# Kernel optimization log

Hardware: AMD Instinct MI355X
Metric: run time of the kernel (lower is better)

The kernel has to match this reference:

```python
import jax, jax.numpy as jnp
import numpy as np

HEAD_SIZE = 64
NEG_INF = float('-inf')


def setup_inputs() -> dict:
    key = jax.random.key(0)
    ks = jax.random.split(key, 4)
    B, S, H, D = 8, 4096, 1024, HEAD_SIZE
    scale = 1.0 / np.sqrt(H)
    return {
        'x': jax.random.normal(ks[0], (B, S, H), dtype=jnp.float32),
        'Wq': jax.random.normal(ks[1], (H, D), dtype=jnp.float32) * scale,
        'bq': jnp.zeros((D,), dtype=jnp.float32),
        'Wk': jax.random.normal(ks[2], (H, D), dtype=jnp.float32) * scale,
        'bk': jnp.zeros((D,), dtype=jnp.float32),
        'Wv': jax.random.normal(ks[3], (H, D), dtype=jnp.float32) * scale,
        'bv': jnp.zeros((D,), dtype=jnp.float32),
    }


def reference(x, Wq, bq, Wk, bk, Wv, bv):
    # x: [B, S, H]; projections -> [B, S, D]
    B, S, H = x.shape
    q = jnp.einsum('bsh,hd->bsd', x, Wq) + bq
    k = jnp.einsum('bsh,hd->bsd', x, Wk) + bk
    v = jnp.einsum('bsh,hd->bsd', x, Wv) + bv
    # raw scores [B, S, S]
    scores = jnp.einsum('bqd,bkd->bqk', q, k)
    # causal mask applied BEFORE scaling (matches original; -inf/scale == -inf)
    causal = jnp.tril(jnp.ones((S, S), dtype=bool))
    scores = jnp.where(causal, scores, NEG_INF)
    scale = 1.0 / jnp.sqrt(jnp.asarray(q.shape[-1], dtype=scores.dtype))
    attn = jax.nn.softmax(scores * scale, axis=-1)
    # dropout = 0.0 (eval) -> identity
    return jnp.einsum('bqk,bkd->bqd', attn, v)
```

## Files before the change

### kernel.cpp

```cpp
#include <hip/hip_runtime.h>
#include <hip/hip_bf16.h>
#include <math.h>

#define SEQ 4096
#define HID 1024
#define DH  64
#define NB  8
#define QSCALE 0.18033688011112042f

typedef unsigned short ushort_t;
typedef unsigned int   uint_t;
typedef __attribute__((ext_vector_type(8))) short  bf16x8;
typedef __attribute__((ext_vector_type(4))) float  f32x4;
typedef __attribute__((ext_vector_type(4))) uint_t u32x4;
typedef __attribute__((ext_vector_type(2))) uint_t u32x2;

static __device__ __forceinline__ ushort_t f2bf(float f) {
    __hip_bfloat16 h = __float2bfloat16(f);
    return *reinterpret_cast<ushort_t*>(&h);
}
static __device__ __forceinline__ ushort_t f2bf_fast(float f) {
    uint_t u = __float_as_uint(f);
    return (ushort_t)((u + 0x8000u) >> 16);
}
static __device__ __forceinline__ uint_t bfpair(float lo, float hi) {
    return (uint_t)f2bf_fast(lo) | ((uint_t)f2bf_fast(hi) << 16);
}

static __device__ __forceinline__ void gld_lds16(const void* g, void* s) {
    __builtin_amdgcn_global_load_lds(
        (const __attribute__((address_space(1))) void*)g,
        (__attribute__((address_space(3))) void*)s, 16, 0, 0);
}

__global__ __launch_bounds__(256) void prep_w(
    const float* __restrict__ Wq, const float* __restrict__ Wk,
    const float* __restrict__ Wv, ushort_t* __restrict__ wts)
{
    __shared__ ushort_t tr[64][72];
    const int bx   = blockIdx.x;
    const int mmat = bx >> 4;
    const int kt   = bx & 15;
    const float* W  = (mmat == 0) ? Wq : (mmat == 1) ? Wk : Wv;
    const float  sc = (mmat == 0) ? QSCALE : 1.0f;

    const int t  = threadIdx.x;
    const int kr = t >> 2, kc = (t & 3) * 16;
    const float* src = W + (size_t)(kt * 64 + kr) * DH + kc;
    float4 a0 = *(const float4*)(src);
    float4 a1 = *(const float4*)(src + 4);
    float4 a2 = *(const float4*)(src + 8);
    float4 a3 = *(const float4*)(src + 12);
    float vv[16] = {a0.x,a0.y,a0.z,a0.w, a1.x,a1.y,a1.z,a1.w,
                    a2.x,a2.y,a2.z,a2.w, a3.x,a3.y,a3.z,a3.w};
    #pragma unroll
    for (int i = 0; i < 16; ++i) tr[kr][kc + i] = f2bf(vv[i] * sc);
    __syncthreads();

    const int cl = t >> 2, jc = (t & 3) * 16;
    const int c  = mmat * 64 + cl;
    ushort_t* dst = wts + kt * 12288 + c * 64;
    #pragma unroll
    for (int jj = 0; jj < 16; ++jj) {
        int j = jc + jj;
        dst[((j >> 3) ^ (cl & 7)) * 8 + (j & 7)] = tr[j][cl];
    }
}

__global__ __launch_bounds__(256) void qkv_proj(
    const float* __restrict__ x, const ushort_t* __restrict__ wts,
    const float* __restrict__ bq, const float* __restrict__ bk,
    const float* __restrict__ bv,
    ushort_t* __restrict__ qimg, ushort_t* __restrict__ kimg,
    ushort_t* __restrict__ vimg)
{
    __shared__ ushort_t xs[2][64][72];
    __shared__ ushort_t bw[2][12288];

    const int t  = threadIdx.x;
    const int w  = t >> 6, l = t & 63, lr = l & 15, lg = l >> 4;
    const int row0 = blockIdx.x * 64;
    const int sxr = t >> 2, sxc = (t & 3) * 16;
    const int ch0 = (lg ^ (lr & 7)) * 8;
    const int ch1 = ((lg + 4) ^ (lr & 7)) * 8;

    f32x4 acc[4][3];
    #pragma unroll
    for (int i = 0; i < 4; ++i)
        #pragma unroll
        for (int j = 0; j < 3; ++j) acc[i][j] = (f32x4){0.f,0.f,0.f,0.f};

    float4 Xf[4];
    u32x4  Bf[6];
    {
        const float* xr = x + (size_t)(row0 + sxr) * HID + sxc;
        Xf[0] = *(const float4*)(xr);      Xf[1] = *(const float4*)(xr + 4);
        Xf[2] = *(const float4*)(xr + 8);  Xf[3] = *(const float4*)(xr + 12);
        const char* bsrc = (const char*)wts + t * 16;
        #pragma unroll
        for (int i = 0; i < 6; ++i) Bf[i] = *(const u32x4*)(bsrc + i * 4096);
    }

    for (int kt = 0; kt < 16; ++kt) {
        const int buf = kt & 1;
        {
            u32x4 p0, p1;
            p0.x = bfpair(Xf[0].x, Xf[0].y);
            p0.y = bfpair(Xf[0].z, Xf[0].w);
            p0.z = bfpair(Xf[1].x, Xf[1].y);
            p0.w = bfpair(Xf[1].z, Xf[1].w);
            p1.x = bfpair(Xf[2].x, Xf[2].y);
            p1.y = bfpair(Xf[2].z, Xf[2].w);
            p1.z = bfpair(Xf[3].x, Xf[3].y);
            p1.w = bfpair(Xf[3].z, Xf[3].w);
            *(u32x4*)&xs[buf][sxr][sxc]     = p0;
            *(u32x4*)&xs[buf][sxr][sxc + 8] = p1;
            char* bdst = (char*)&bw[buf][0] + t * 16;
            #pragma unroll
            for (int i = 0; i < 6; ++i) *(u32x4*)(bdst + i * 4096) = Bf[i];
        }
        __syncthreads();
        if (kt < 15) {
            const float* xr = x + (size_t)(row0 + sxr) * HID + (kt + 1) * 64 + sxc;
            Xf[0] = *(const float4*)(xr);      Xf[1] = *(const float4*)(xr + 4);
            Xf[2] = *(const float4*)(xr + 8);  Xf[3] = *(const float4*)(xr + 12);
            const char* bsrc = (const char*)wts + (kt + 1) * 24576 + t * 16;
            #pragma unroll
            for (int i = 0; i < 6; ++i) Bf[i] = *(const u32x4*)(bsrc + i * 4096);
        }
        bf16x8 af0[4], af1[4];
        #pragma unroll
        for (int rt = 0; rt < 4; ++rt) {
            af0[rt] = *(bf16x8*)&xs[buf][rt * 16 + lr][lg * 8];
            af1[rt] = *(bf16x8*)&xs[buf][rt * 16 + lr][lg * 8 + 32];
        }
        #pragma unroll
        for (int ctl = 0; ctl < 3; ++ctl) {
            const int c = (w * 3 + ctl) * 16 + lr;
            bf16x8 b0 = *(bf16x8*)&bw[buf][c * 64 + ch0];
            bf16x8 b1 = *(bf16x8*)&bw[buf][c * 64 + ch1];
            #pragma unroll
            for (int rt = 0; rt < 4; ++rt) {
                acc[rt][ctl] = __builtin_amdgcn_mfma_f32_16x16x32_bf16(
                    af0[rt], b0, acc[rt][ctl], 0, 0, 0);
                acc[rt][ctl] = __builtin_amdgcn_mfma_f32_16x16x32_bf16(
                    af1[rt], b1, acc[rt][ctl], 0, 0, 0);
            }
        }
    }

    #pragma unroll
    for (int ctl = 0; ctl < 3; ++ctl) {
        const int c    = (w * 3 + ctl) * 16 + lr;
        const int mmat = c >> 6;
        const int cc   = c & 63;
        const float* bp = (mmat == 0) ? bq : (mmat == 1) ? bk : bv;
        const float bias = bp[cc] * (mmat == 0 ? QSCALE : 1.0f);
        #pragma unroll
        for (int rt = 0; rt < 4; ++rt)
            #pragma unroll
            for (int r = 0; r < 4; ++r) {
                const int s = row0 + rt * 16 + lg * 4 + r;
                const ushort_t v = f2bf(acc[rt][ctl][r] + bias);
                if (mmat == 0)
                    qimg[(size_t)s * 64 + cc] = v;
                else if (mmat == 1)
                    kimg[(size_t)(s >> 6) * 4096 + (s & 63) * 64 +
                         ((cc >> 3) ^ (s & 7)) * 8 + (cc & 7)] = v;
                else
                    vimg[(size_t)(s >> 6) * 4096 + (size_t)cc * 64 +
                         (((s & 63) >> 3) ^ (cc & 7)) * 8 + (s & 7)] = v;
            }
    }
}

__global__ __launch_bounds__(256) void attn(
    const ushort_t* __restrict__ qimg, const ushort_t* __restrict__ kimg,
    const ushort_t* __restrict__ vimg, float* __restrict__ outg)
{
    __shared__ ushort_t kvs[2][8192];
    __shared__ ushort_t ps[64][72];

    const int t  = threadIdx.x;
    const int w  = t >> 6, l = t & 63, lr = l & 15, g = l >> 4;
    const int bx = blockIdx.x;
    const int qt = (bx < 256) ? (63 - (bx >> 3)) : ((bx - 256) >> 3);
    const int b  = bx & 7;
    const int q0 = qt * 64;
    const int ch0 = (g ^ (lr & 7)) * 8;
    const int ch1 = ((g + 4) ^ (lr & 7)) * 8;
    const int qq  = q0 + w * 16 + lr;

    bf16x8 qf0, qf1;
    {
        const ushort_t* qp = qimg + (size_t)(b * SEQ + qq) * 64 + g * 8;
        qf0 = *(const bf16x8*)(qp);
        qf1 = *(const bf16x8*)(qp + 32);
    }

    f32x4 o[4];
    #pragma unroll
    for (int dt = 0; dt < 4; ++dt) o[dt] = (f32x4){0.f,0.f,0.f,0.f};
    float lpart = 0.f;

    const char* kbase = (const char*)kimg + (size_t)b * 524288;
    const char* vbase = (const char*)vimg + (size_t)b * 524288;
    const int wo = w * 1024;
    const int lo = l * 16;

    {
        char* lk = (char*)&kvs[0][0];
        gld_lds16(kbase + wo + lo,        lk + wo);
        gld_lds16(kbase + wo + lo + 4096, lk + wo + 4096);
        gld_lds16(vbase + wo + lo,        lk + wo + 8192);
        gld_lds16(vbase + wo + lo + 4096, lk + wo + 12288);
    }

    for (int kt = 0; kt <= qt; ++kt) {
        const int cur = kt & 1;
        __syncthreads();
        if (kt < qt) {
            const char* ks = kbase + (size_t)(kt + 1) * 8192;
            const char* vs = vbase + (size_t)(kt + 1) * 8192;
            char*       lk = (char*)&kvs[cur ^ 1][0];
            gld_lds16(ks + wo + lo,        lk + wo);
            gld_lds16(ks + wo + lo + 4096, lk + wo + 4096);
            gld_lds16(vs + wo + lo,        lk + wo + 8192);
            gld_lds16(vs + wo + lo + 4096, lk + wo + 12288);
        }

        const ushort_t* kb = &kvs[cur][0];
        f32x4 s[4];
        #pragma unroll
        for (int ct = 0; ct < 4; ++ct) {
            const int rowb = (ct * 16 + lr) * 64;
            bf16x8 kf0 = *(const bf16x8*)(kb + rowb + ch0);
            bf16x8 kf1 = *(const bf16x8*)(kb + rowb + ch1);
            s[ct] = (f32x4){0.f,0.f,0.f,0.f};
            s[ct] = __builtin_amdgcn_mfma_f32_16x16x32_bf16(kf0, qf0, s[ct], 0, 0, 0);
            s[ct] = __builtin_amdgcn_mfma_f32_16x16x32_bf16(kf1, qf1, s[ct], 0, 0, 0);
        }

        if (kt == qt) {
            const int kvb = kt * 64 + g * 4;
            #pragma unroll
            for (int ct = 0; ct < 4; ++ct) {
                float p0 = ((kvb + ct*16 + 0) > qq) ? 0.f : __builtin_amdgcn_exp2f(s[ct][0]);
                float p1 = ((kvb + ct*16 + 1) > qq) ? 0.f : __builtin_amdgcn_exp2f(s[ct][1]);
                float p2 = ((kvb + ct*16 + 2) > qq) ? 0.f : __builtin_amdgcn_exp2f(s[ct][2]);
                float p3 = ((kvb + ct*16 + 3) > qq) ? 0.f : __builtin_amdgcn_exp2f(s[ct][3]);
                lpart += (p0 + p1) + (p2 + p3);
                u32x2 pk = { bfpair(p0, p1), bfpair(p2, p3) };
                *(u32x2*)&ps[w * 16 + lr][ct * 16 + g * 4] = pk;
            }
        } else {
            #pragma unroll
            for (int ct = 0; ct < 4; ++ct) {
                float p0 = __builtin_amdgcn_exp2f(s[ct][0]);
                float p1 = __builtin_amdgcn_exp2f(s[ct][1]);
                float p2 = __builtin_amdgcn_exp2f(s[ct][2]);
                float p3 = __builtin_amdgcn_exp2f(s[ct][3]);
                lpart += (p0 + p1) + (p2 + p3);
                u32x2 pk = { bfpair(p0, p1), bfpair(p2, p3) };
                *(u32x2*)&ps[w * 16 + lr][ct * 16 + g * 4] = pk;
            }
        }
        asm volatile("s_waitcnt lgkmcnt(0)" ::: "memory");

        bf16x8 pf0 = *(const bf16x8*)&ps[w * 16 + lr][g * 8];
        bf16x8 pf1 = *(const bf16x8*)&ps[w * 16 + lr][32 + g * 8];
        const ushort_t* vb = &kvs[cur][4096];
        #pragma unroll
        for (int dt = 0; dt < 4; ++dt) {
            const int rowb = (dt * 16 + lr) * 64;
            bf16x8 vf0 = *(const bf16x8*)(vb + rowb + ch0);
            bf16x8 vf1 = *(const bf16x8*)(vb + rowb + ch1);
            o[dt] = __builtin_amdgcn_mfma_f32_16x16x32_bf16(vf0, pf0, o[dt], 0, 0, 0);
            o[dt] = __builtin_amdgcn_mfma_f32_16x16x32_bf16(vf1, pf1, o[dt], 0, 0, 0);
        }
    }

    lpart += __shfl_xor(lpart, 16);
    lpart += __shfl_xor(lpart, 32);
    const float inv = 1.0f / lpart;

    float* orow = outg + (size_t)(b * SEQ + qq) * 64;
    #pragma unroll
    for (int dt = 0; dt < 4; ++dt) {
        float4 val = { o[dt][0] * inv, o[dt][1] * inv,
                       o[dt][2] * inv, o[dt][3] * inv };
        *(float4*)&orow[dt * 16 + g * 4] = val;
    }
}

extern "C" void kernel_launch(void* const* d_in, const int* in_sizes, int n_in,
                              void* d_out, int out_size, void* d_ws, size_t ws_size,
                              hipStream_t stream) {
    const float* x  = (const float*)d_in[0];
    const float* Wq = (const float*)d_in[1];
    const float* bq = (const float*)d_in[2];
    const float* Wk = (const float*)d_in[3];
    const float* bk = (const float*)d_in[4];
    const float* Wv = (const float*)d_in[5];
    const float* bv = (const float*)d_in[6];
    float* out = (float*)d_out;

    const size_t per = (size_t)NB * SEQ * DH;
    ushort_t* q   = (ushort_t*)d_ws;
    ushort_t* k   = q + per;
    ushort_t* v   = k + per;
    ushort_t* wts = v + per;

    prep_w  <<<dim3(48),  256, 0, stream>>>(Wq, Wk, Wv, wts);
    qkv_proj<<<dim3(512), 256, 0, stream>>>(x, wts, bq, bk, bv, q, k, v);
    attn    <<<dim3(512), 256, 0, stream>>>(q, k, v, out);
}
```

Before: 273.4 us.

## Split attention key range across two blocks and merge partials; async weight loads

The attention kernel now splits each query tile's causal key range into two halves, each handled by a separate block (1024 blocks). Each block writes unnormalised partial outputs and row sums to workspace, and a new merge kernel adds them and normalises. The aim is better load balance and more parallelism across CUs for the long causal rows. The cost is an extra launch and extra partial-buffer traffic. Separately, the projection kernel loads weights with direct global-to-LDS copies instead of staging them in registers, and uses a cheaper bf16 rounding in its epilogue. The merge relies on a fixed softmax offset with no running max, which the code before also used, so adding the two halves' sums is consistent.

```diff
diff --git a/kernel.cpp b/kernel.cpp
--- a/kernel.cpp
+++ b/kernel.cpp
@@ -90,15 +90,18 @@
         #pragma unroll
         for (int j = 0; j < 3; ++j) acc[i][j] = (f32x4){0.f,0.f,0.f,0.f};
 
+    const char* wbase = (const char*)wts;
+    const int   wlo   = w * 1024 + l * 16;
+
     float4 Xf[4];
-    u32x4  Bf[6];
     {
         const float* xr = x + (size_t)(row0 + sxr) * HID + sxc;
         Xf[0] = *(const float4*)(xr);      Xf[1] = *(const float4*)(xr + 4);
         Xf[2] = *(const float4*)(xr + 8);  Xf[3] = *(const float4*)(xr + 12);
-        const char* bsrc = (const char*)wts + t * 16;
-        #pragma unroll
-        for (int i = 0; i < 6; ++i) Bf[i] = *(const u32x4*)(bsrc + i * 4096);
+        char* bdst = (char*)&bw[0][0] + w * 1024;
+        #pragma unroll
+        for (int i = 0; i < 6; ++i)
+            gld_lds16(wbase + wlo + i * 4096, bdst + i * 4096);
     }
 
     for (int kt = 0; kt < 16; ++kt) {
@@ -115,18 +118,17 @@
             p1.w = bfpair(Xf[3].z, Xf[3].w);
             *(u32x4*)&xs[buf][sxr][sxc]     = p0;
             *(u32x4*)&xs[buf][sxr][sxc + 8] = p1;
-            char* bdst = (char*)&bw[buf][0] + t * 16;
-            #pragma unroll
-            for (int i = 0; i < 6; ++i) *(u32x4*)(bdst + i * 4096) = Bf[i];
         }
         __syncthreads();
         if (kt < 15) {
             const float* xr = x + (size_t)(row0 + sxr) * HID + (kt + 1) * 64 + sxc;
             Xf[0] = *(const float4*)(xr);      Xf[1] = *(const float4*)(xr + 4);
             Xf[2] = *(const float4*)(xr + 8);  Xf[3] = *(const float4*)(xr + 12);
-            const char* bsrc = (const char*)wts + (kt + 1) * 24576 + t * 16;
-            #pragma unroll
-            for (int i = 0; i < 6; ++i) Bf[i] = *(const u32x4*)(bsrc + i * 4096);
+            char* bdst = (char*)&bw[buf ^ 1][0] + w * 1024;
+            const char* bsrc = wbase + (size_t)(kt + 1) * 24576 + wlo;
+            #pragma unroll
+            for (int i = 0; i < 6; ++i)
+                gld_lds16(bsrc + i * 4096, bdst + i * 4096);
         }
         bf16x8 af0[4], af1[4];
         #pragma unroll
@@ -161,7 +163,7 @@
             #pragma unroll
             for (int r = 0; r < 4; ++r) {
                 const int s = row0 + rt * 16 + lg * 4 + r;
-                const ushort_t v = f2bf(acc[rt][ctl][r] + bias);
+                const ushort_t v = f2bf_fast(acc[rt][ctl][r] + bias);
                 if (mmat == 0)
                     qimg[(size_t)s * 64 + cc] = v;
                 else if (mmat == 1)
@@ -176,17 +178,23 @@
 
 __global__ __launch_bounds__(256) void attn(
     const ushort_t* __restrict__ qimg, const ushort_t* __restrict__ kimg,
-    const ushort_t* __restrict__ vimg, float* __restrict__ outg)
+    const ushort_t* __restrict__ vimg,
+    float* __restrict__ Opart, float* __restrict__ Lpart)
 {
     __shared__ ushort_t kvs[2][8192];
     __shared__ ushort_t ps[64][72];
 
     const int t  = threadIdx.x;
     const int w  = t >> 6, l = t & 63, lr = l & 15, g = l >> 4;
-    const int bx = blockIdx.x;
-    const int qt = (bx < 256) ? (63 - (bx >> 3)) : ((bx - 256) >> 3);
-    const int b  = bx & 7;
-    const int q0 = qt * 64;
+    const int bx   = blockIdx.x;
+    const int half = bx & 1;
+    const int u    = bx >> 1;
+    const int qt   = 63 - (u >> 3);
+    const int b    = u & 7;
+    const int q0   = qt * 64;
+    const int n    = qt + 1, h = n >> 1;
+    const int t0   = half ? h : 0;
+    const int t1   = half ? n : h;
     const int ch0 = (g ^ (lr & 7)) * 8;
     const int ch1 = ((g + 4) ^ (lr & 7)) * 8;
     const int qq  = q0 + w * 16 + lr;
@@ -208,18 +216,20 @@
     const int wo = w * 1024;
     const int lo = l * 16;
 
-    {
+    if (t0 < t1) {
+        const char* ks = kbase + (size_t)t0 * 8192;
+        const char* vs = vbase + (size_t)t0 * 8192;
         char* lk = (char*)&kvs[0][0];
-        gld_lds16(kbase + wo + lo,        lk + wo);
-        gld_lds16(kbase + wo + lo + 4096, lk + wo + 4096);
-        gld_lds16(vbase + wo + lo,        lk + wo + 8192);
-        gld_lds16(vbase + wo + lo + 4096, lk + wo + 12288);
-    }
-
-    for (int kt = 0; kt <= qt; ++kt) {
-        const int cur = kt & 1;
+        gld_lds16(ks + wo + lo,        lk + wo);
+        gld_lds16(ks + wo + lo + 4096, lk + wo + 4096);
+        gld_lds16(vs + wo + lo,        lk + wo + 8192);
+        gld_lds16(vs + wo + lo + 4096, lk + wo + 12288);
+    }
+
+    for (int kt = t0; kt < t1; ++kt) {
+        const int cur = (kt - t0) & 1;
         __syncthreads();
-        if (kt < qt) {
+        if (kt + 1 < t1) {
             const char* ks = kbase + (size_t)(kt + 1) * 8192;
             const char* vs = vbase + (size_t)(kt + 1) * 8192;
             char*       lk = (char*)&kvs[cur ^ 1][0];
@@ -282,14 +292,38 @@
 
     lpart += __shfl_xor(lpart, 16);
     lpart += __shfl_xor(lpart, 32);
-    const float inv = 1.0f / lpart;
-
-    float* orow = outg + (size_t)(b * SEQ + qq) * 64;
-    #pragma unroll
-    for (int dt = 0; dt < 4; ++dt) {
-        float4 val = { o[dt][0] * inv, o[dt][1] * inv,
-                       o[dt][2] * inv, o[dt][3] * inv };
-        *(float4*)&orow[dt * 16 + g * 4] = val;
+
+    const int m = b * 64 + qt;
+    float* Op = Opart + ((size_t)half * 512 + m) * 4096;
+    #pragma unroll
+    for (int dt = 0; dt < 4; ++dt)
+        *(f32x4*)&Op[(w * 16 + lr) * 64 + dt * 16 + g * 4] = o[dt];
+    if (g == 0)
+        Lpart[((size_t)half * 512 + m) * 64 + w * 16 + lr] = lpart;
+}
+
+__global__ __launch_bounds__(256) void merge_o(
+    const float* __restrict__ Opart, const float* __restrict__ Lpart,
+    float* __restrict__ outg)
+{
+    const int m = blockIdx.x;
+    const int b = m >> 6, qt = m & 63;
+    const int t = threadIdx.x;
+    const int row = t >> 2, c = (t & 3) * 16;
+
+    const float* A = Opart + (size_t)m * 4096 + row * 64 + c;
+    const float* B = Opart + (size_t)(512 + m) * 4096 + row * 64 + c;
+    const float la = Lpart[(size_t)m * 64 + row];
+    const float lb = Lpart[(size_t)(512 + m) * 64 + row];
+    const float inv = 1.0f / (la + lb);
+    float* dst = outg + ((size_t)b * SEQ + qt * 64 + row) * 64 + c;
+    #pragma unroll
+    for (int j = 0; j < 4; ++j) {
+        float4 va = *(const float4*)(A + j * 4);
+        float4 vb = *(const float4*)(B + j * 4);
+        float4 vo = { (va.x + vb.x) * inv, (va.y + vb.y) * inv,
+                      (va.z + vb.z) * inv, (va.w + vb.w) * inv };
+        *(float4*)(dst + j * 4) = vo;
     }
 }
 
@@ -310,8 +344,11 @@
     ushort_t* k   = q + per;
     ushort_t* v   = k + per;
     ushort_t* wts = v + per;
-
-    prep_w  <<<dim3(48),  256, 0, stream>>>(Wq, Wk, Wv, wts);
-    qkv_proj<<<dim3(512), 256, 0, stream>>>(x, wts, bq, bk, bv, q, k, v);
-    attn    <<<dim3(512), 256, 0, stream>>>(q, k, v, out);
-}
+    float* Opart  = (float*)((char*)d_ws + (size_t)(16u << 20));
+    float* Lpart  = (float*)((char*)d_ws + (size_t)(40u << 20));
+
+    prep_w  <<<dim3(48),   256, 0, stream>>>(Wq, Wk, Wv, wts);
+    qkv_proj<<<dim3(512),  256, 0, stream>>>(x, wts, bq, bk, bv, q, k, v);
+    attn    <<<dim3(1024), 256, 0, stream>>>(q, k, v, Opart, Lpart);
+    merge_o <<<dim3(512),  256, 0, stream>>>(Opart, Lpart, out);
+}
```

New measurement: 259.0 us. 1.06x faster.
